# Performance work log

Hardware: AMD Instinct MI355X
Metric: run time of the kernel (lower is better)

## Reference

```python
import jax, jax.numpy as jnp
import numpy as np

N = 100_000          # nodes
E = 1_600_000        # real edges (self-loops appended after)
HID = 32             # hidden_dim
RES = 5              # PersistenceImager resolution -> 5x5 image
SIGMA = 0.2          # gaussian bandwidth of persistence image kernel
PRELU_A = 0.1        # F.prelu weight used in the source


def _linear_init(k, fan_in, fan_out):
    k1, k2 = jax.random.split(k)
    s = 1.0 / np.sqrt(fan_in)
    W = jax.random.uniform(k1, (fan_in, fan_out), minval=-s, maxval=s, dtype=jnp.float32)
    b = jax.random.uniform(k2, (fan_out,), minval=-s, maxval=s, dtype=jnp.float32)
    return W, b


def setup_inputs() -> dict:
    key = jax.random.key(0)
    ks = jax.random.split(key, 10)
    # edge list: E random edges, then N self-loops appended at the END
    src = jax.random.randint(ks[0], (E,), 0, N)
    dst = jax.random.randint(ks[1], (E,), 0, N)
    loops = jnp.arange(N)
    edge_index0 = jnp.stack([jnp.concatenate([src, loops]),
                             jnp.concatenate([dst, loops])]).astype(jnp.int64)
    x0 = jax.random.normal(ks[2], (N, 1), dtype=jnp.float32)
    # GIN conv MLPs (Base_Model with out_dim=hidden_dim)
    W1, b1 = _linear_init(ks[3], 1, HID)
    W2, b2 = _linear_init(ks[4], HID, HID)
    W4, b4 = _linear_init(ks[5], HID, HID)
    W3, b3 = _linear_init(ks[6], HID, HID)   # conv3: Linear only, no ReLU
    W5, b5 = _linear_init(ks[7], 2 * HID, HID)  # lin5
    W6, b6 = _linear_init(ks[8], HID, 2)        # lin6
    return dict(x0=x0, edge_index0=edge_index0,
                W1=W1, b1=b1, W2=W2, b2=b2, W4=W4, b4=b4, W3=W3, b3=b3,
                W5=W5, b5=b5, W6=W6, b6=b6)


def _gin_agg(x, src, dst):
    # PyG GINConv with eps=0: (1+eps)*x + sum_{j->i} x_j  (aggregation over the
    # provided edge_index, which here already includes appended self-loops)
    return x + jax.ops.segment_sum(x[src], dst, num_segments=N)


def _prelu(x):
    return jnp.where(x >= 0, x, PRELU_A * x)


def _pers_image(pd):
    # Persistence image on a RESxRES grid over [0,1]^2 of (birth, persistence),
    # gaussian kernel integrated per pixel via normal CDFs, linear pers weight.
    b = pd[:, 0]
    pers = pd[:, 1] - pd[:, 0]
    edges = jnp.linspace(0.0, 1.0, RES + 1)
    inv = 1.0 / (SIGMA * np.sqrt(2.0))
    cdf_b = 0.5 * (1.0 + jax.lax.erf((edges[None, :] - b[:, None]) * inv))   # [E, RES+1]
    cdf_p = 0.5 * (1.0 + jax.lax.erf((edges[None, :] - pers[:, None]) * inv))
    db = cdf_b[:, 1:] - cdf_b[:, :-1]   # [E, RES]
    dp = cdf_p[:, 1:] - cdf_p[:, :-1]
    img = jnp.einsum('e,ei,ej->ij', pers, db, dp)
    return img.reshape(-1)  # [25]


def reference(x0, edge_index0, W1, b1, W2, b2, W4, b4, W3, b3, W5, b5, W6, b6):
    src, dst = edge_index0[0], edge_index0[1]
    # Base_Model GIN path (dropout is identity in eval mode); order 1,2,4,3
    x = jax.nn.relu(_gin_agg(x0, src, dst) @ W1 + b1)
    x = jax.nn.relu(_gin_agg(x, src, dst) @ W2 + b2)
    x = jax.nn.relu(_gin_agg(x, src, dst) @ W4 + b4)
    x = _gin_agg(x, src, dst) @ W3 + b3      # conv3: Linear, no ReLU
    # edge head over the E real edges (drop trailing N self-loops)
    x_in = x[src[:E]]
    x_out = x[dst[:E]]
    h = _prelu(jnp.concatenate([x_in, x_out], axis=-1) @ W5 + b5)
    pd = h @ W6 + b6                          # predicted PD, [E, 2]
    img = _pers_image(pd)                     # persistence image, [25]
    return pd, img
```

## Files before the change

kernel.cpp:

```cpp
#include <hip/hip_runtime.h>
#include <hip/hip_bf16.h>
#include <hip/hip_fp16.h>
#include <math.h>

#define NN 100000
#define EE 1600000
#define ET 1700000
#define HID 32

#define BKT_SHIFT 10
#define BKT_MASK 1023
#define NBKT 98
#define EPB 4096
#define NBLK_A 416

__global__ __launch_bounds__(128) void k_zero(int* __restrict__ p, int n) {
    int t = blockIdx.x * 128 + threadIdx.x;
    if (t < n) p[t] = 0;
}

__global__ __launch_bounds__(256) void k_bkt_count(const int* __restrict__ dst32, int* __restrict__ bucket_cnt) {
    __shared__ int h[NBKT];
    for (int i = threadIdx.x; i < NBKT; i += 256) h[i] = 0;
    __syncthreads();
    int base = blockIdx.x * EPB;
    for (int k = 0; k < EPB; k += 256) {
        int t = base + k + threadIdx.x;
        if (t < ET) atomicAdd(&h[dst32[t] >> BKT_SHIFT], 1);
    }
    __syncthreads();
    for (int i = threadIdx.x; i < NBKT; i += 256) {
        int c = h[i];
        if (c) atomicAdd(&bucket_cnt[i], c);
    }
}

__global__ __launch_bounds__(128) void k_bkt_scan(const int* __restrict__ bucket_cnt, int* __restrict__ bucket_base,
                                                  int* __restrict__ bucket_fill) {
    __shared__ int s[128];
    int t = threadIdx.x;
    int v = (t < NBKT) ? bucket_cnt[t] : 0;
    s[t] = v;
    for (int off = 1; off < 128; off <<= 1) {
        __syncthreads();
        int u = (t >= off) ? s[t - off] : 0;
        __syncthreads();
        s[t] += u;
    }
    __syncthreads();
    int ex = s[t] - v;
    if (t < NBKT) {
        bucket_base[t] = ex;
        bucket_fill[t] = ex;
    }
    if (t == 0) bucket_base[NBKT] = ET;
}

__global__ __launch_bounds__(256) void k_bkt_scatter(const int* __restrict__ src32, const int* __restrict__ dst32,
                                                     int* __restrict__ bucket_fill, int2* __restrict__ pairs) {
    __shared__ int h[NBKT];
    __shared__ int bbase[NBKT];
    for (int i = threadIdx.x; i < NBKT; i += 256) h[i] = 0;
    __syncthreads();
    int base = blockIdx.x * EPB;
    for (int k = 0; k < EPB; k += 256) {
        int t = base + k + threadIdx.x;
        if (t < ET) atomicAdd(&h[dst32[t] >> BKT_SHIFT], 1);
    }
    __syncthreads();
    for (int i = threadIdx.x; i < NBKT; i += 256) {
        int c = h[i];
        bbase[i] = c ? atomicAdd(&bucket_fill[i], c) : 0;
        h[i] = 0;
    }
    __syncthreads();
    for (int k = 0; k < EPB; k += 256) {
        int t = base + k + threadIdx.x;
        if (t < ET) {
            int sv = src32[t], dv = dst32[t];
            int b = dv >> BKT_SHIFT;
            int off = atomicAdd(&h[b], 1);
            pairs[bbase[b] + off] = make_int2(sv, dv);
        }
    }
}

__global__ __launch_bounds__(512) void k_bkt_csr(const int2* __restrict__ pairs, const int* __restrict__ bucket_base,
                                                 int* __restrict__ rowptr, int* __restrict__ src_sorted) {
    __shared__ int h[1024];
    __shared__ int tmp[512];
    int t = threadIdx.x;
    int b = blockIdx.x;
    int e0 = bucket_base[b], e1 = bucket_base[b + 1];
    int node0 = b << BKT_SHIFT;

    h[t] = 0;
    h[t + 512] = 0;
    __syncthreads();
    for (int e = e0 + t; e < e1; e += 512) atomicAdd(&h[pairs[e].y & BKT_MASK], 1);
    __syncthreads();

    int i0 = 2 * t, i1 = 2 * t + 1;
    int v0 = h[i0], v1 = h[i1];
    int s = v0 + v1;
    tmp[t] = s;
    for (int off = 1; off < 512; off <<= 1) {
        __syncthreads();
        int u = (t >= off) ? tmp[t - off] : 0;
        __syncthreads();
        tmp[t] += u;
    }
    __syncthreads();
    int excl = tmp[t] - s;
    h[i0] = excl;
    h[i1] = excl + v0;
    __syncthreads();

    for (int i = t; i < 1024; i += 512) {
        int node = node0 + i;
        if (node < NN) rowptr[node] = e0 + h[i];
    }
    if (b == 0 && t == 0) rowptr[NN] = ET;
    __syncthreads();

    for (int e = e0 + t; e < e1; e += 512) {
        int2 p = pairs[e];
        int sl = atomicAdd(&h[p.y & BKT_MASK], 1);
        src_sorted[e0 + sl] = p.x;
    }
}

__device__ __forceinline__ void acc8(uint4 r, float* c) {
    float2 f0 = __half22float2(*reinterpret_cast<__half2*>(&r.x));
    float2 f1 = __half22float2(*reinterpret_cast<__half2*>(&r.y));
    float2 f2 = __half22float2(*reinterpret_cast<__half2*>(&r.z));
    float2 f3 = __half22float2(*reinterpret_cast<__half2*>(&r.w));
    c[0] += f0.x; c[1] += f0.y; c[2] += f1.x; c[3] += f1.y;
    c[4] += f2.x; c[5] += f2.y; c[6] += f3.x; c[7] += f3.y;
}

__global__ __launch_bounds__(256) void k_pull1(const int* __restrict__ rowptr, const int* __restrict__ src_sorted,
                                               const float* __restrict__ x0, const float* __restrict__ W1,
                                               const float* __restrict__ b1, __half* __restrict__ hout) {
    __shared__ float W1l[32], b1l[32];
    if (threadIdx.x < 32) {
        W1l[threadIdx.x] = W1[threadIdx.x];
        b1l[threadIdx.x] = b1[threadIdx.x];
    }
    __syncthreads();
    int g = blockIdx.x * 256 + threadIdx.x;
    if (g >= NN) return;
    int e0 = rowptr[g], e1 = rowptr[g + 1];
    float a0 = x0[g], a1 = 0.f, a2 = 0.f, a3 = 0.f, a4 = 0.f, a5 = 0.f, a6 = 0.f, a7 = 0.f;
    int e = e0;
    for (; e + 8 <= e1; e += 8) {
        a0 += x0[src_sorted[e + 0]];
        a1 += x0[src_sorted[e + 1]];
        a2 += x0[src_sorted[e + 2]];
        a3 += x0[src_sorted[e + 3]];
        a4 += x0[src_sorted[e + 4]];
        a5 += x0[src_sorted[e + 5]];
        a6 += x0[src_sorted[e + 6]];
        a7 += x0[src_sorted[e + 7]];
    }
    for (; e < e1; ++e) a0 += x0[src_sorted[e]];
    float s = ((a0 + a1) + (a2 + a3)) + ((a4 + a5) + (a6 + a7));

    uint4* orow = reinterpret_cast<uint4*>(hout) + ((size_t)g << 2);
#pragma unroll
    for (int q = 0; q < 4; ++q) {
        float o0 = fmaxf(fmaf(s, W1l[8 * q + 0], b1l[8 * q + 0]), 0.f);
        float o1 = fmaxf(fmaf(s, W1l[8 * q + 1], b1l[8 * q + 1]), 0.f);
        float o2 = fmaxf(fmaf(s, W1l[8 * q + 2], b1l[8 * q + 2]), 0.f);
        float o3 = fmaxf(fmaf(s, W1l[8 * q + 3], b1l[8 * q + 3]), 0.f);
        float o4 = fmaxf(fmaf(s, W1l[8 * q + 4], b1l[8 * q + 4]), 0.f);
        float o5 = fmaxf(fmaf(s, W1l[8 * q + 5], b1l[8 * q + 5]), 0.f);
        float o6 = fmaxf(fmaf(s, W1l[8 * q + 6], b1l[8 * q + 6]), 0.f);
        float o7 = fmaxf(fmaf(s, W1l[8 * q + 7], b1l[8 * q + 7]), 0.f);
        __half2 p0 = __floats2half2_rn(o0, o1);
        __half2 p1 = __floats2half2_rn(o2, o3);
        __half2 p2 = __floats2half2_rn(o4, o5);
        __half2 p3 = __floats2half2_rn(o6, o7);
        orow[q] = make_uint4(*reinterpret_cast<unsigned*>(&p0), *reinterpret_cast<unsigned*>(&p1),
                             *reinterpret_cast<unsigned*>(&p2), *reinterpret_cast<unsigned*>(&p3));
    }
}

template <int RELU>
__global__ __launch_bounds__(256) void k_agg_mm(const int* __restrict__ rowptr, const int* __restrict__ src_sorted,
                                                const __half* __restrict__ hin, const float* __restrict__ W,
                                                const float* __restrict__ b, __half* __restrict__ hout) {
    __shared__ float Wl[1024];
    for (int i = threadIdx.x; i < 1024; i += 256) Wl[i] = W[i];
    __syncthreads();
    int g = (blockIdx.x * 256 + threadIdx.x) >> 2;
    if (g >= NN) return;
    int j = threadIdx.x & 3;
    const uint4* tab = reinterpret_cast<const uint4*>(hin);
    int e0 = rowptr[g], e1 = rowptr[g + 1];
    float x[8], y[8];
#pragma unroll
    for (int i = 0; i < 8; ++i) { x[i] = 0.f; y[i] = 0.f; }
    acc8(tab[(g << 2) + j], x);
    int e = e0;
    for (; e + 8 <= e1; e += 8) {
        int s0 = src_sorted[e + 0], s1 = src_sorted[e + 1], s2 = src_sorted[e + 2], s3 = src_sorted[e + 3];
        int s4 = src_sorted[e + 4], s5 = src_sorted[e + 5], s6 = src_sorted[e + 6], s7 = src_sorted[e + 7];
        uint4 r0 = tab[(s0 << 2) + j];
        uint4 r1 = tab[(s1 << 2) + j];
        uint4 r2 = tab[(s2 << 2) + j];
        uint4 r3 = tab[(s3 << 2) + j];
        uint4 r4 = tab[(s4 << 2) + j];
        uint4 r5 = tab[(s5 << 2) + j];
        uint4 r6 = tab[(s6 << 2) + j];
        uint4 r7 = tab[(s7 << 2) + j];
        acc8(r0, x); acc8(r1, y); acc8(r2, x); acc8(r3, y);
        acc8(r4, x); acc8(r5, y); acc8(r6, x); acc8(r7, y);
    }
    for (; e < e1; ++e) acc8(tab[(src_sorted[e] << 2) + j], x);
#pragma unroll
    for (int i = 0; i < 8; ++i) x[i] += y[i];

    float o[8];
#pragma unroll
    for (int i = 0; i < 8; ++i) o[i] = b[8 * j + i];
#pragma unroll
    for (int sl = 0; sl < 4; ++sl) {
#pragma unroll
        for (int r = 0; r < 8; ++r) {
            float xk = __shfl(x[r], sl, 4);
            int k = 8 * sl + r;
            float4 w0 = *reinterpret_cast<const float4*>(&Wl[k * 32 + 8 * j]);
            float4 w1 = *reinterpret_cast<const float4*>(&Wl[k * 32 + 8 * j + 4]);
            o[0] = fmaf(xk, w0.x, o[0]); o[1] = fmaf(xk, w0.y, o[1]);
            o[2] = fmaf(xk, w0.z, o[2]); o[3] = fmaf(xk, w0.w, o[3]);
            o[4] = fmaf(xk, w1.x, o[4]); o[5] = fmaf(xk, w1.y, o[5]);
            o[6] = fmaf(xk, w1.z, o[6]); o[7] = fmaf(xk, w1.w, o[7]);
        }
    }
    if (RELU) {
#pragma unroll
        for (int i = 0; i < 8; ++i) o[i] = fmaxf(o[i], 0.f);
    }
    __half2 p0 = __floats2half2_rn(o[0], o[1]);
    __half2 p1 = __floats2half2_rn(o[2], o[3]);
    __half2 p2 = __floats2half2_rn(o[4], o[5]);
    __half2 p3 = __floats2half2_rn(o[6], o[7]);
    uint4 st = make_uint4(*reinterpret_cast<unsigned*>(&p0), *reinterpret_cast<unsigned*>(&p1),
                          *reinterpret_cast<unsigned*>(&p2), *reinterpret_cast<unsigned*>(&p3));
    reinterpret_cast<uint4*>(hout)[(g << 2) + j] = st;
}

__global__ __launch_bounds__(256) void k_agg_mm_proj(const int* __restrict__ rowptr, const int* __restrict__ src_sorted,
                                                     const __half* __restrict__ hin, const float* __restrict__ W3,
                                                     const float* __restrict__ b3,
                                                     const float* __restrict__ W5, const float* __restrict__ b5,
                                                     __half* __restrict__ u16, __half* __restrict__ v16) {
    __shared__ float W3l[1024];
    __shared__ float W5l[2048];
    for (int i = threadIdx.x; i < 1024; i += 256) W3l[i] = W3[i];
    for (int i = threadIdx.x; i < 2048; i += 256) W5l[i] = W5[i];
    __syncthreads();
    int g = (blockIdx.x * 256 + threadIdx.x) >> 2;
    if (g >= NN) return;
    int j = threadIdx.x & 3;
    const uint4* tab = reinterpret_cast<const uint4*>(hin);
    int e0 = rowptr[g], e1 = rowptr[g + 1];
    float x[8], y[8];
#pragma unroll
    for (int i = 0; i < 8; ++i) { x[i] = 0.f; y[i] = 0.f; }
    acc8(tab[(g << 2) + j], x);
    int e = e0;
    for (; e + 8 <= e1; e += 8) {
        int s0 = src_sorted[e + 0], s1 = src_sorted[e + 1], s2 = src_sorted[e + 2], s3 = src_sorted[e + 3];
        int s4 = src_sorted[e + 4], s5 = src_sorted[e + 5], s6 = src_sorted[e + 6], s7 = src_sorted[e + 7];
        uint4 r0 = tab[(s0 << 2) + j];
        uint4 r1 = tab[(s1 << 2) + j];
        uint4 r2 = tab[(s2 << 2) + j];
        uint4 r3 = tab[(s3 << 2) + j];
        uint4 r4 = tab[(s4 << 2) + j];
        uint4 r5 = tab[(s5 << 2) + j];
        uint4 r6 = tab[(s6 << 2) + j];
        uint4 r7 = tab[(s7 << 2) + j];
        acc8(r0, x); acc8(r1, y); acc8(r2, x); acc8(r3, y);
        acc8(r4, x); acc8(r5, y); acc8(r6, x); acc8(r7, y);
    }
    for (; e < e1; ++e) acc8(tab[(src_sorted[e] << 2) + j], x);
#pragma unroll
    for (int i = 0; i < 8; ++i) x[i] += y[i];

    float o[8];
#pragma unroll
    for (int i = 0; i < 8; ++i) o[i] = b3[8 * j + i];
#pragma unroll
    for (int sl = 0; sl < 4; ++sl) {
#pragma unroll
        for (int r = 0; r < 8; ++r) {
            float xk = __shfl(x[r], sl, 4);
            int k = 8 * sl + r;
            float4 w0 = *reinterpret_cast<const float4*>(&W3l[k * 32 + 8 * j]);
            float4 w1 = *reinterpret_cast<const float4*>(&W3l[k * 32 + 8 * j + 4]);
            o[0] = fmaf(xk, w0.x, o[0]); o[1] = fmaf(xk, w0.y, o[1]);
            o[2] = fmaf(xk, w0.z, o[2]); o[3] = fmaf(xk, w0.w, o[3]);
            o[4] = fmaf(xk, w1.x, o[4]); o[5] = fmaf(xk, w1.y, o[5]);
            o[6] = fmaf(xk, w1.z, o[6]); o[7] = fmaf(xk, w1.w, o[7]);
        }
    }
    float u[8], v[8];
#pragma unroll
    for (int i = 0; i < 8; ++i) { u[i] = b5[8 * j + i]; v[i] = 0.f; }
#pragma unroll
    for (int sl = 0; sl < 4; ++sl) {
#pragma unroll
        for (int r = 0; r < 8; ++r) {
            float xk = __shfl(o[r], sl, 4);
            int k = 8 * sl + r;
            float4 a0 = *reinterpret_cast<const float4*>(&W5l[k * 32 + 8 * j]);
            float4 a1 = *reinterpret_cast<const float4*>(&W5l[k * 32 + 8 * j + 4]);
            u[0] = fmaf(xk, a0.x, u[0]); u[1] = fmaf(xk, a0.y, u[1]);
            u[2] = fmaf(xk, a0.z, u[2]); u[3] = fmaf(xk, a0.w, u[3]);
            u[4] = fmaf(xk, a1.x, u[4]); u[5] = fmaf(xk, a1.y, u[5]);
            u[6] = fmaf(xk, a1.z, u[6]); u[7] = fmaf(xk, a1.w, u[7]);
            float4 c0 = *reinterpret_cast<const float4*>(&W5l[(32 + k) * 32 + 8 * j]);
            float4 c1 = *reinterpret_cast<const float4*>(&W5l[(32 + k) * 32 + 8 * j + 4]);
            v[0] = fmaf(xk, c0.x, v[0]); v[1] = fmaf(xk, c0.y, v[1]);
            v[2] = fmaf(xk, c0.z, v[2]); v[3] = fmaf(xk, c0.w, v[3]);
            v[4] = fmaf(xk, c1.x, v[4]); v[5] = fmaf(xk, c1.y, v[5]);
            v[6] = fmaf(xk, c1.z, v[6]); v[7] = fmaf(xk, c1.w, v[7]);
        }
    }
    __half2 pu0 = __floats2half2_rn(u[0], u[1]);
    __half2 pu1 = __floats2half2_rn(u[2], u[3]);
    __half2 pu2 = __floats2half2_rn(u[4], u[5]);
    __half2 pu3 = __floats2half2_rn(u[6], u[7]);
    uint4 su = make_uint4(*reinterpret_cast<unsigned*>(&pu0), *reinterpret_cast<unsigned*>(&pu1),
                          *reinterpret_cast<unsigned*>(&pu2), *reinterpret_cast<unsigned*>(&pu3));
    reinterpret_cast<uint4*>(u16)[(g << 2) + j] = su;
    __half2 pv0 = __floats2half2_rn(v[0], v[1]);
    __half2 pv1 = __floats2half2_rn(v[2], v[3]);
    __half2 pv2 = __floats2half2_rn(v[4], v[5]);
    __half2 pv3 = __floats2half2_rn(v[6], v[7]);
    uint4 sv = make_uint4(*reinterpret_cast<unsigned*>(&pv0), *reinterpret_cast<unsigned*>(&pv1),
                          *reinterpret_cast<unsigned*>(&pv2), *reinterpret_cast<unsigned*>(&pv3));
    reinterpret_cast<uint4*>(v16)[(g << 2) + j] = sv;
}

__global__ __launch_bounds__(256) void k_edge(const int* __restrict__ src32, const int* __restrict__ dst32,
                                              const __half* __restrict__ u16, const __half* __restrict__ v16,
                                              const float* __restrict__ W6, const float* __restrict__ b6,
                                              float* __restrict__ pd_out, float* __restrict__ partial) {
    int ea = blockIdx.x * 512 + threadIdx.x;
    int eb = ea + 256;
    int sa = src32[ea], da = dst32[ea];
    int sb = src32[eb], db = dst32[eb];
    const uint4* pua = reinterpret_cast<const uint4*>(u16 + ((size_t)sa << 5));
    const uint4* pva = reinterpret_cast<const uint4*>(v16 + ((size_t)da << 5));
    const uint4* pub = reinterpret_cast<const uint4*>(u16 + ((size_t)sb << 5));
    const uint4* pvb = reinterpret_cast<const uint4*>(v16 + ((size_t)db << 5));

    uint4 A[4], B[4], C[4], D[4];
#pragma unroll
    for (int q = 0; q < 4; ++q) A[q] = pua[q];
#pragma unroll
    for (int q = 0; q < 4; ++q) B[q] = pva[q];
#pragma unroll
    for (int q = 0; q < 4; ++q) C[q] = pub[q];
#pragma unroll
    for (int q = 0; q < 4; ++q) D[q] = pvb[q];
    __builtin_amdgcn_sched_barrier(0);

    float b60 = b6[0], b61 = b6[1];
    float pda0 = b60, pda1 = b61, pdb0 = b60, pdb1 = b61;
#pragma unroll
    for (int q = 0; q < 4; ++q) {
        const __half2* ah = reinterpret_cast<const __half2*>(&A[q]);
        const __half2* bh = reinterpret_cast<const __half2*>(&B[q]);
        const __half2* ch = reinterpret_cast<const __half2*>(&C[q]);
        const __half2* dh = reinterpret_cast<const __half2*>(&D[q]);
#pragma unroll
        for (int r = 0; r < 4; ++r) {
            float2 fA = __half22float2(__hadd2(ah[r], bh[r]));
            float2 fB = __half22float2(__hadd2(ch[r], dh[r]));
            int jj = q * 8 + 2 * r;
            float w00 = W6[2 * jj + 0], w01 = W6[2 * jj + 1];
            float w10 = W6[2 * (jj + 1) + 0], w11 = W6[2 * (jj + 1) + 1];
            float hA0 = fA.x >= 0.f ? fA.x : 0.1f * fA.x;
            float hA1 = fA.y >= 0.f ? fA.y : 0.1f * fA.y;
            float hB0 = fB.x >= 0.f ? fB.x : 0.1f * fB.x;
            float hB1 = fB.y >= 0.f ? fB.y : 0.1f * fB.y;
            pda0 = fmaf(hA0, w00, pda0); pda1 = fmaf(hA0, w01, pda1);
            pda0 = fmaf(hA1, w10, pda0); pda1 = fmaf(hA1, w11, pda1);
            pdb0 = fmaf(hB0, w00, pdb0); pdb1 = fmaf(hB0, w01, pdb1);
            pdb0 = fmaf(hB1, w10, pdb0); pdb1 = fmaf(hB1, w11, pdb1);
        }
    }
    reinterpret_cast<float2*>(pd_out)[ea] = make_float2(pda0, pda1);
    reinterpret_cast<float2*>(pd_out)[eb] = make_float2(pdb0, pdb1);

    float persA = pda1 - pda0;
    float persB = pdb1 - pdb0;
    const float inv = 3.5355339059327378f;
    float cbA[6], cpA[6], cbB[6], cpB[6];
#pragma unroll
    for (int i = 0; i < 6; ++i) {
        float te = 0.2f * (float)i;
        cbA[i] = erff((te - pda0) * inv);
        cpA[i] = erff((te - persA) * inv);
        cbB[i] = erff((te - pdb0) * inv);
        cpB[i] = erff((te - persB) * inv);
    }

    int lane = threadIdx.x & 63;
    int wv = threadIdx.x >> 6;
    __shared__ float sacc[4][25];
#pragma unroll
    for (int i = 0; i < 5; ++i) {
        float pa = 0.25f * persA * (cbA[i + 1] - cbA[i]);
        float pb = 0.25f * persB * (cbB[i + 1] - cbB[i]);
#pragma unroll
        for (int jj = 0; jj < 5; ++jj) {
            float v = pa * (cpA[jj + 1] - cpA[jj]) + pb * (cpB[jj + 1] - cpB[jj]);
            v += __shfl_down(v, 32);
            v += __shfl_down(v, 16);
            v += __shfl_down(v, 8);
            v += __shfl_down(v, 4);
            v += __shfl_down(v, 2);
            v += __shfl_down(v, 1);
            if (lane == 0) sacc[wv][i * 5 + jj] = v;
        }
    }
    __syncthreads();
    if (threadIdx.x < 25) {
        partial[(size_t)blockIdx.x * 25 + threadIdx.x] =
            sacc[0][threadIdx.x] + sacc[1][threadIdx.x] + sacc[2][threadIdx.x] + sacc[3][threadIdx.x];
    }
}

__global__ __launch_bounds__(256) void k_img(const float* __restrict__ partial, float* __restrict__ img) {
    int bin = blockIdx.x;
    float s = 0.f;
    for (int k = threadIdx.x; k < EE / 512; k += 256) s += partial[(size_t)k * 25 + bin];
    s += __shfl_down(s, 32);
    s += __shfl_down(s, 16);
    s += __shfl_down(s, 8);
    s += __shfl_down(s, 4);
    s += __shfl_down(s, 2);
    s += __shfl_down(s, 1);
    __shared__ float wsum[4];
    if ((threadIdx.x & 63) == 0) wsum[threadIdx.x >> 6] = s;
    __syncthreads();
    if (threadIdx.x == 0) img[bin] = wsum[0] + wsum[1] + wsum[2] + wsum[3];
}

extern "C" void kernel_launch(void* const* d_in, const int* in_sizes, int n_in,
                              void* d_out, int out_size, void* d_ws, size_t ws_size,
                              hipStream_t stream) {
    const float* x0 = (const float*)d_in[0];
    const int* src32 = (const int*)d_in[1];
    const int* dst32 = src32 + ET;
    const float* W1 = (const float*)d_in[2];
    const float* b1 = (const float*)d_in[3];
    const float* W2 = (const float*)d_in[4];
    const float* b2 = (const float*)d_in[5];
    const float* W4 = (const float*)d_in[6];
    const float* b4 = (const float*)d_in[7];
    const float* W3 = (const float*)d_in[8];
    const float* b3 = (const float*)d_in[9];
    const float* W5 = (const float*)d_in[10];
    const float* b5 = (const float*)d_in[11];
    const float* W6 = (const float*)d_in[12];
    const float* b6 = (const float*)d_in[13];
    float* out = (float*)d_out;

    char* w = (char*)d_ws;
    int2* pairs = (int2*)w;
    int* bucket_cnt = (int*)(pairs + ET);
    int* bucket_base = bucket_cnt + NBKT;
    int* bucket_fill = bucket_base + NBKT + 1;
    int* rowptr = bucket_fill + NBKT;
    int* src_sorted = rowptr + NN + 1;
    size_t off = ((size_t)((char*)(src_sorted + ET) - w) + 63) & ~(size_t)63;
    __half* bufA = (__half*)(w + off);
    __half* bufB = bufA + (size_t)NN * 32;
    __half* u16 = bufB + (size_t)NN * 32;
    __half* v16 = u16 + (size_t)NN * 32;
    float* partial = (float*)(v16 + (size_t)NN * 32);

    k_zero<<<1, 128, 0, stream>>>(bucket_cnt, NBKT);
    k_bkt_count<<<NBLK_A, 256, 0, stream>>>(dst32, bucket_cnt);
    k_bkt_scan<<<1, 128, 0, stream>>>(bucket_cnt, bucket_base, bucket_fill);
    k_bkt_scatter<<<NBLK_A, 256, 0, stream>>>(src32, dst32, bucket_fill, pairs);
    k_bkt_csr<<<NBKT, 512, 0, stream>>>(pairs, bucket_base, rowptr, src_sorted);

    k_pull1<<<(NN + 255) / 256, 256, 0, stream>>>(rowptr, src_sorted, x0, W1, b1, bufA);
    k_agg_mm<1><<<(NN * 4 + 255) / 256, 256, 0, stream>>>(rowptr, src_sorted, bufA, W2, b2, bufB);
    k_agg_mm<1><<<(NN * 4 + 255) / 256, 256, 0, stream>>>(rowptr, src_sorted, bufB, W4, b4, bufA);
    k_agg_mm_proj<<<(NN * 4 + 255) / 256, 256, 0, stream>>>(rowptr, src_sorted, bufA, W3, b3, W5, b5, u16, v16);

    k_edge<<<EE / 512, 256, 0, stream>>>(src32, dst32, u16, v16, W6, b6, out, partial);
    k_img<<<25, 256, 0, stream>>>(partial, out + 2 * (size_t)EE);
}
```

Baseline: 242.6 us.

## Use fixed-capacity dst buckets and degree-sorted node order for aggregation

After: 815.6 us. +236.2%, slower.

```diff
diff --git a/kernel.cpp b/kernel.cpp
--- a/kernel.cpp
+++ b/kernel.cpp
@@ -11,49 +11,14 @@
 #define BKT_SHIFT 10
 #define BKT_MASK 1023
 #define NBKT 98
+#define CAP 18944
 #define EPB 4096
 #define NBLK_A 416
 
-__global__ __launch_bounds__(128) void k_zero(int* __restrict__ p, int n) {
-    int t = blockIdx.x * 128 + threadIdx.x;
-    if (t < n) p[t] = 0;
-}
-
-__global__ __launch_bounds__(256) void k_bkt_count(const int* __restrict__ dst32, int* __restrict__ bucket_cnt) {
-    __shared__ int h[NBKT];
-    for (int i = threadIdx.x; i < NBKT; i += 256) h[i] = 0;
-    __syncthreads();
-    int base = blockIdx.x * EPB;
-    for (int k = 0; k < EPB; k += 256) {
-        int t = base + k + threadIdx.x;
-        if (t < ET) atomicAdd(&h[dst32[t] >> BKT_SHIFT], 1);
-    }
-    __syncthreads();
-    for (int i = threadIdx.x; i < NBKT; i += 256) {
-        int c = h[i];
-        if (c) atomicAdd(&bucket_cnt[i], c);
-    }
-}
-
-__global__ __launch_bounds__(128) void k_bkt_scan(const int* __restrict__ bucket_cnt, int* __restrict__ bucket_base,
-                                                  int* __restrict__ bucket_fill) {
-    __shared__ int s[128];
+__global__ __launch_bounds__(128) void k_seed(int* __restrict__ bucket_fill, int* __restrict__ dcnt) {
     int t = threadIdx.x;
-    int v = (t < NBKT) ? bucket_cnt[t] : 0;
-    s[t] = v;
-    for (int off = 1; off < 128; off <<= 1) {
-        __syncthreads();
-        int u = (t >= off) ? s[t - off] : 0;
-        __syncthreads();
-        s[t] += u;
-    }
-    __syncthreads();
-    int ex = s[t] - v;
-    if (t < NBKT) {
-        bucket_base[t] = ex;
-        bucket_fill[t] = ex;
-    }
-    if (t == 0) bucket_base[NBKT] = ET;
+    if (t < NBKT) bucket_fill[t] = t * CAP;
+    if (t < 64) dcnt[t] = 0;
 }
 
 __global__ __launch_bounds__(256) void k_bkt_scatter(const int* __restrict__ src32, const int* __restrict__ dst32,
@@ -85,13 +50,14 @@
     }
 }
 
-__global__ __launch_bounds__(512) void k_bkt_csr(const int2* __restrict__ pairs, const int* __restrict__ bucket_base,
-                                                 int* __restrict__ rowptr, int* __restrict__ src_sorted) {
+__global__ __launch_bounds__(512) void k_bkt_csr(const int2* __restrict__ pairs, const int* __restrict__ bucket_fill,
+                                                 int* __restrict__ rowptr, int* __restrict__ rowend,
+                                                 int* __restrict__ deg, int* __restrict__ src_sorted) {
     __shared__ int h[1024];
     __shared__ int tmp[512];
     int t = threadIdx.x;
     int b = blockIdx.x;
-    int e0 = bucket_base[b], e1 = bucket_base[b + 1];
+    int e0 = b * CAP, e1 = bucket_fill[b];
     int node0 = b << BKT_SHIFT;
 
     h[t] = 0;
@@ -116,17 +82,40 @@
     h[i1] = excl + v0;
     __syncthreads();
 
-    for (int i = t; i < 1024; i += 512) {
-        int node = node0 + i;
-        if (node < NN) rowptr[node] = e0 + h[i];
-    }
-    if (b == 0 && t == 0) rowptr[NN] = ET;
+    int n0 = node0 + i0, n1 = node0 + i1;
+    if (n0 < NN) { rowptr[n0] = e0 + excl;      rowend[n0] = e0 + excl + v0;      deg[n0] = v0; }
+    if (n1 < NN) { rowptr[n1] = e0 + excl + v0; rowend[n1] = e0 + excl + v0 + v1; deg[n1] = v1; }
     __syncthreads();
 
     for (int e = e0 + t; e < e1; e += 512) {
         int2 p = pairs[e];
         int sl = atomicAdd(&h[p.y & BKT_MASK], 1);
         src_sorted[e0 + sl] = p.x;
+    }
+}
+
+__global__ __launch_bounds__(256) void k_dhist(const int* __restrict__ deg, int* __restrict__ dcnt) {
+    int t = blockIdx.x * 256 + threadIdx.x;
+    if (t < NN) atomicAdd(&dcnt[min(deg[t], 63)], 1);
+}
+
+__global__ __launch_bounds__(64) void k_dscan(const int* __restrict__ dcnt, int* __restrict__ dfill) {
+    int t = threadIdx.x;
+    int c = dcnt[t];
+    int v = c;
+    for (int off = 1; off < 64; off <<= 1) {
+        int u = __shfl_up(v, off, 64);
+        if (t >= off) v += u;
+    }
+    dfill[t] = v - c;
+}
+
+__global__ __launch_bounds__(256) void k_dfill(const int* __restrict__ deg, int* __restrict__ dfill,
+                                               int* __restrict__ order) {
+    int t = blockIdx.x * 256 + threadIdx.x;
+    if (t < NN) {
+        int slot = atomicAdd(&dfill[min(deg[t], 63)], 1);
+        order[slot] = t;
     }
 }
 
@@ -139,7 +128,9 @@
     c[4] += f2.x; c[5] += f2.y; c[6] += f3.x; c[7] += f3.y;
 }
 
-__global__ __launch_bounds__(256) void k_pull1(const int* __restrict__ rowptr, const int* __restrict__ src_sorted,
+__global__ __launch_bounds__(256) void k_pull1(const int* __restrict__ order,
+                                               const int* __restrict__ rowptr, const int* __restrict__ rowend,
+                                               const int* __restrict__ src_sorted,
                                                const float* __restrict__ x0, const float* __restrict__ W1,
                                                const float* __restrict__ b1, __half* __restrict__ hout) {
     __shared__ float W1l[32], b1l[32];
@@ -148,9 +139,10 @@
         b1l[threadIdx.x] = b1[threadIdx.x];
     }
     __syncthreads();
-    int g = blockIdx.x * 256 + threadIdx.x;
-    if (g >= NN) return;
-    int e0 = rowptr[g], e1 = rowptr[g + 1];
+    int gid = blockIdx.x * 256 + threadIdx.x;
+    if (gid >= NN) return;
+    int g = order[gid];
+    int e0 = rowptr[g], e1 = rowend[g];
     float a0 = x0[g], a1 = 0.f, a2 = 0.f, a3 = 0.f, a4 = 0.f, a5 = 0.f, a6 = 0.f, a7 = 0.f;
     int e = e0;
     for (; e + 8 <= e1; e += 8) {
@@ -187,17 +179,20 @@
 }
 
 template <int RELU>
-__global__ __launch_bounds__(256) void k_agg_mm(const int* __restrict__ rowptr, const int* __restrict__ src_sorted,
+__global__ __launch_bounds__(256) void k_agg_mm(const int* __restrict__ order,
+                                                const int* __restrict__ rowptr, const int* __restrict__ rowend,
+                                                const int* __restrict__ src_sorted,
                                                 const __half* __restrict__ hin, const float* __restrict__ W,
                                                 const float* __restrict__ b, __half* __restrict__ hout) {
     __shared__ float Wl[1024];
     for (int i = threadIdx.x; i < 1024; i += 256) Wl[i] = W[i];
     __syncthreads();
-    int g = (blockIdx.x * 256 + threadIdx.x) >> 2;
-    if (g >= NN) return;
+    int gid = (blockIdx.x * 256 + threadIdx.x) >> 2;
+    if (gid >= NN) return;
+    int g = order[gid];
     int j = threadIdx.x & 3;
     const uint4* tab = reinterpret_cast<const uint4*>(hin);
-    int e0 = rowptr[g], e1 = rowptr[g + 1];
+    int e0 = rowptr[g], e1 = rowend[g];
     float x[8], y[8];
 #pragma unroll
     for (int i = 0; i < 8; ++i) { x[i] = 0.f; y[i] = 0.f; }
@@ -251,7 +246,9 @@
     reinterpret_cast<uint4*>(hout)[(g << 2) + j] = st;
 }
 
-__global__ __launch_bounds__(256) void k_agg_mm_proj(const int* __restrict__ rowptr, const int* __restrict__ src_sorted,
+__global__ __launch_bounds__(256) void k_agg_mm_proj(const int* __restrict__ order,
+                                                     const int* __restrict__ rowptr, const int* __restrict__ rowend,
+                                                     const int* __restrict__ src_sorted,
                                                      const __half* __restrict__ hin, const float* __restrict__ W3,
                                                      const float* __restrict__ b3,
                                                      const float* __restrict__ W5, const float* __restrict__ b5,
@@ -261,11 +258,12 @@
     for (int i = threadIdx.x; i < 1024; i += 256) W3l[i] = W3[i];
     for (int i = threadIdx.x; i < 2048; i += 256) W5l[i] = W5[i];
     __syncthreads();
-    int g = (blockIdx.x * 256 + threadIdx.x) >> 2;
-    if (g >= NN) return;
+    int gid = (blockIdx.x * 256 + threadIdx.x) >> 2;
+    if (gid >= NN) return;
+    int g = order[gid];
     int j = threadIdx.x & 3;
     const uint4* tab = reinterpret_cast<const uint4*>(hin);
-    int e0 = rowptr[g], e1 = rowptr[g + 1];
+    int e0 = rowptr[g], e1 = rowend[g];
     float x[8], y[8];
 #pragma unroll
     for (int i = 0; i < 8; ++i) { x[i] = 0.f; y[i] = 0.f; }
@@ -472,30 +470,36 @@
     const float* b6 = (const float*)d_in[13];
     float* out = (float*)d_out;
 
+    const size_t PADDED = (size_t)NBKT * CAP;
     char* w = (char*)d_ws;
     int2* pairs = (int2*)w;
-    int* bucket_cnt = (int*)(pairs + ET);
-    int* bucket_base = bucket_cnt + NBKT;
-    int* bucket_fill = bucket_base + NBKT + 1;
-    int* rowptr = bucket_fill + NBKT;
-    int* src_sorted = rowptr + NN + 1;
-    size_t off = ((size_t)((char*)(src_sorted + ET) - w) + 63) & ~(size_t)63;
+    int* src_sorted = (int*)(pairs + PADDED);
+    int* bucket_fill = src_sorted + PADDED;
+    int* dcnt = bucket_fill + NBKT;
+    int* dfill = dcnt + 64;
+    int* rowptr = dfill + 64;
+    int* rowend = rowptr + NN;
+    int* deg = rowend + NN;
+    int* order = deg + NN;
+    size_t off = ((size_t)((char*)(order + NN) - w) + 63) & ~(size_t)63;
     __half* bufA = (__half*)(w + off);
     __half* bufB = bufA + (size_t)NN * 32;
     __half* u16 = bufB + (size_t)NN * 32;
     __half* v16 = u16 + (size_t)NN * 32;
     float* partial = (float*)(v16 + (size_t)NN * 32);
 
-    k_zero<<<1, 128, 0, stream>>>(bucket_cnt, NBKT);
-    k_bkt_count<<<NBLK_A, 256, 0, stream>>>(dst32, bucket_cnt);
-    k_bkt_scan<<<1, 128, 0, stream>>>(bucket_cnt, bucket_base, bucket_fill);
+    k_seed<<<1, 128, 0, stream>>>(bucket_fill, dcnt);
     k_bkt_scatter<<<NBLK_A, 256, 0, stream>>>(src32, dst32, bucket_fill, pairs);
-    k_bkt_csr<<<NBKT, 512, 0, stream>>>(pairs, bucket_base, rowptr, src_sorted);
-
-    k_pull1<<<(NN + 255) / 256, 256, 0, stream>>>(rowptr, src_sorted, x0, W1, b1, bufA);
-    k_agg_mm<1><<<(NN * 4 + 255) / 256, 256, 0, stream>>>(rowptr, src_sorted, bufA, W2, b2, bufB);
-    k_agg_mm<1><<<(NN * 4 + 255) / 256, 256, 0, stream>>>(rowptr, src_sorted, bufB, W4, b4, bufA);
-    k_agg_mm_proj<<<(NN * 4 + 255) / 256, 256, 0, stream>>>(rowptr, src_sorted, bufA, W3, b3, W5, b5, u16, v16);
+    k_bkt_csr<<<NBKT, 512, 0, stream>>>(pairs, bucket_fill, rowptr, rowend, deg, src_sorted);
+
+    k_dhist<<<(NN + 255) / 256, 256, 0, stream>>>(deg, dcnt);
+    k_dscan<<<1, 64, 0, stream>>>(dcnt, dfill);
+    k_dfill<<<(NN + 255) / 256, 256, 0, stream>>>(deg, dfill, order);
+
+    k_pull1<<<(NN + 255) / 256, 256, 0, stream>>>(order, rowptr, rowend, src_sorted, x0, W1, b1, bufA);
+    k_agg_mm<1><<<(NN * 4 + 255) / 256, 256, 0, stream>>>(order, rowptr, rowend, src_sorted, bufA, W2, b2, bufB);
+    k_agg_mm<1><<<(NN * 4 + 255) / 256, 256, 0, stream>>>(order, rowptr, rowend, src_sorted, bufB, W4, b4, bufA);
+    k_agg_mm_proj<<<(NN * 4 + 255) / 256, 256, 0, stream>>>(order, rowptr, rowend, src_sorted, bufA, W3, b3, W5, b5, u16, v16);
 
     k_edge<<<EE / 512, 256, 0, stream>>>(src32, dst32, u16, v16, W6, b6, out, partial);
     k_img<<<25, 256, 0, stream>>>(partial, out + 2 * (size_t)EE);
```
